# Performance work log

Hardware: AMD Instinct MI355X
Metric: run time of the kernel (lower is better)

The kernel has to match this reference:

```python
import jax, jax.numpy as jnp
import numpy as np
from jax import lax

BN_EPS = 1e-5  # eval-mode BatchNorm with running_mean=0, running_var=1


def _interp_mat(n_in, n_out):
    # align_corners=True bilinear interpolation matrix [n_out, n_in]
    if n_out == 1:
        coords = np.zeros((1,))
    else:
        coords = np.arange(n_out) * (n_in - 1) / (n_out - 1)
    lo = np.clip(np.floor(coords).astype(np.int64), 0, max(n_in - 2, 0))
    frac = (coords - lo).astype(np.float32)
    M = np.zeros((n_out, n_in), dtype=np.float32)
    M[np.arange(n_out), lo] += 1.0 - frac
    if n_in > 1:
        M[np.arange(n_out), lo + 1] += frac
    return jnp.asarray(M)


def _resize_ac(x, H, W):
    # bilinear, align_corners=True, over trailing two dims
    Mh = _interp_mat(x.shape[-2], H)
    Mw = _interp_mat(x.shape[-1], W)
    return jnp.einsum('...hw,Hh,Ww->...HW', x, Mh, Mw)


def _conv(x, w, b, pad):
    y = lax.conv_general_dilated(x, w, (1, 1), [(pad, pad), (pad, pad)],
                                 dimension_numbers=('NCHW', 'OIHW', 'NCHW'))
    return y + b[None, :, None, None]


def setup_inputs() -> dict:
    key = jax.random.key(0)
    ks = jax.random.split(key, 16)
    C, KD, VD, NCLS, BS = 256, 32, 128, 10, 4
    sizes = [64, 32, 16, 8, 4]
    inp = {}
    for l, s in enumerate(sizes):
        inp[f'feat{l}'] = jax.random.normal(ks[l], (BS, C, s, s), jnp.float32)
    inp['attentions'] = jax.random.normal(ks[5], (NCLS, C, 16, 16), jnp.float32)

    def w(k, shape):
        return jax.random.normal(k, shape, jnp.float32) * 0.05

    inp['key_t_w'] = w(ks[6], (KD, C, 3, 3)); inp['key_t_b'] = jnp.zeros((KD,), jnp.float32)
    inp['value_t_w'] = w(ks[7], (VD, C, 3, 3)); inp['value_t_b'] = jnp.zeros((VD,), jnp.float32)
    inp['key_q_w'] = w(ks[8], (5, KD, C, 3, 3)); inp['key_q_b'] = jnp.zeros((5, KD), jnp.float32)
    inp['value_q_w'] = w(ks[9], (5, VD, C, 3, 3)); inp['value_q_b'] = jnp.zeros((5, VD), jnp.float32)
    inp['bn_gamma'] = jnp.ones((5, 256), jnp.float32)
    inp['bn_beta'] = jnp.zeros((5, 256), jnp.float32)
    inp['combine_w'] = w(ks[10], (256, 512, 1, 1)); inp['combine_b'] = jnp.zeros((256,), jnp.float32)
    return inp


def reference(feat0, feat1, feat2, feat3, feat4, attentions,
              key_t_w, key_t_b, value_t_w, value_t_b,
              key_q_w, key_q_b, value_q_w, value_q_b,
              bn_gamma, bn_beta, combine_w, combine_b):
    feats = [feat0, feat1, feat2, feat3, feat4]
    ncls, _, h, w_ = attentions.shape
    hw = h * w_
    kt = _conv(attentions, key_t_w, key_t_b, 1).reshape(ncls, 32, hw)   # [n,32,hw]
    vt = _conv(attentions, value_t_w, value_t_b, 1).reshape(ncls, 128, hw)  # [n,128,hw]
    bn_scale = bn_gamma * np.float32(1.0 / np.sqrt(1.0 + BN_EPS))
    outs, fas = [], []
    for l, f in enumerate(feats):
        bs, _, H, W = f.shape
        fr = _resize_ac(f, h, w_)                                        # [b,C,h,w]
        kq = _conv(fr, key_q_w[l], key_q_b[l], 1).reshape(bs, 32, hw)    # [b,32,hw]
        vq = _conv(fr, value_q_w[l], value_q_b[l], 1)                    # [b,128,h,w]
        # p[b,n,i,j] = sum_k kq[b,k,i] * kt[n,k,j]; softmax over i (torch dim=1)
        p = jnp.einsum('bki,nkj->bnij', kq, kt)
        p = jax.nn.softmax(p, axis=2)
        # full attention maps: channels = template pixel j, spatial = query pixel i
        fa = _resize_ac(jnp.swapaxes(p, 2, 3).reshape(bs, ncls, hw, h, w_), H, W)
        # val_t_out summed over classes: sum_n sum_i vt[n,c,i] * p[b,n,i,j]
        agg = jnp.einsum('nci,bnij->bcj', vt, p).reshape(bs, 128, h, w_)
        final = jnp.concatenate([ncls * vq, agg], axis=1)                # [b,256,h,w]
        final = _resize_ac(final, H, W)
        final = final * bn_scale[l][None, :, None, None] + bn_beta[l][None, :, None, None]
        outs.append(_conv(jnp.concatenate([f, final], axis=1), combine_w, combine_b, 0))
        fas.append(fa)
    return (*outs, *fas)
```

## Files before the change

### kernel.cpp

```cpp
#include <hip/hip_runtime.h>

constexpr int CIN   = 256;
constexpr int KD    = 32;
constexpr int VD    = 128;
constexpr int NCLS  = 10;
constexpr int BS    = 4;
constexpr int HW    = 256;
constexpr float BNC = 0.9999950000374997f;

typedef unsigned short u16;
typedef __attribute__((ext_vector_type(8))) __bf16 bf8v;
typedef __attribute__((ext_vector_type(4))) float f4v;

static __device__ __forceinline__ int imin(int a, int b) { return a < b ? a : b; }

static __device__ __forceinline__ u16 f2bf(float v) {
  union { float f; unsigned u; } x; x.f = v;
  unsigned r = x.u + 0x7FFFu + ((x.u >> 16) & 1u);
  return (u16)(r >> 16);
}
static __device__ __forceinline__ float bf2f(u16 h) {
  union { unsigned u; float f; } x; x.u = ((unsigned)h) << 16;
  return x.f;
}

static __device__ __forceinline__ f4v mfma16(bf8v a, bf8v b, f4v c) {
  return __builtin_amdgcn_mfma_f32_16x16x32_bf16(a, b, c, 0, 0, 0);
}

__constant__ const int c_jbase[5] = {0, 16384, 20480, 21504, 21760};

__global__ __launch_bounds__(256) void k_prep1(
    const float* __restrict__ f0, const float* __restrict__ f1,
    const float* __restrict__ f2, const float* __restrict__ f3,
    const float* __restrict__ f4, const float* __restrict__ att,
    const float* __restrict__ vqw, const float* __restrict__ vtw,
    const float* __restrict__ kqw, const float* __restrict__ ktw,
    const float* __restrict__ cw, const float* __restrict__ gamma,
    const float* __restrict__ cbias, const float* __restrict__ beta,
    u16* __restrict__ Xf, u16* __restrict__ Xr,
    u16* __restrict__ Awv, u16* __restrict__ Awk,
    u16* __restrict__ cwA, u16* __restrict__ cw2A, float* __restrict__ cb) {
  __shared__ float sm[16][65];
  int blk = blockIdx.x;
  int tid = threadIdx.x;
  if (blk < 384) {
    const float* fin; u16* dstbase; int SS, px0;
    if (blk < 344) {
      int l, base, nb;
      if (blk < 256)      { l = 0; base = 0;   nb = 64; }
      else if (blk < 320) { l = 1; base = 256; nb = 16; }
      else if (blk < 336) { l = 2; base = 320; nb = 4; }
      else if (blk < 340) { l = 3; base = 336; nb = 1; }
      else                { l = 4; base = 340; nb = 1; }
      int local = blk - base;
      int b = local / nb, chunk = local % nb;
      int S = 64 >> l; SS = S * S;
      px0 = chunk * 64;
      fin = (l == 0 ? f0 : l == 1 ? f1 : l == 2 ? f2 : l == 3 ? f3 : f4)
            + (size_t)b * CIN * SS;
      dstbase = Xf + (size_t)(c_jbase[l] + b * SS) * 512;
    } else {
      int a = blk - 344;
      int imgA = a >> 2, chunk = a & 3;
      SS = 256; px0 = chunk * 64;
      fin = att + (size_t)imgA * CIN * 256;
      dstbase = Xr + (size_t)(20 + imgA) * 131072;
    }
    int px_r = tid & 63, cr = tid >> 6;
    int px_w = tid >> 2, c4 = (tid & 3) * 4;
    for (int cbk = 0; cbk < 16; ++cbk) {
      __syncthreads();
#pragma unroll
      for (int q = 0; q < 4; ++q) {
        int cl = q * 4 + cr;
        float v = 0.f;
        if (px0 + px_r < SS) v = fin[(size_t)(cbk * 16 + cl) * SS + px0 + px_r];
        sm[cl][px_r] = v;
      }
      __syncthreads();
      if (px0 + px_w < SS) {
        u16 hh[4], ll[4];
#pragma unroll
        for (int e = 0; e < 4; ++e) {
          float v = sm[c4 + e][px_w];
          hh[e] = f2bf(v); ll[e] = f2bf(v - bf2f(hh[e]));
        }
        uint2 wh, wl;
        wh.x = (unsigned)hh[0] | ((unsigned)hh[1] << 16); wh.y = (unsigned)hh[2] | ((unsigned)hh[3] << 16);
        wl.x = (unsigned)ll[0] | ((unsigned)ll[1] << 16); wl.y = (unsigned)ll[2] | ((unsigned)ll[3] << 16);
        u16* dst = dstbase + (size_t)(px0 + px_w) * 512 + cbk * 16 + c4;
        *reinterpret_cast<uint2*>(dst) = wh;
        *reinterpret_cast<uint2*>(dst + 256) = wl;
      }
    }
  } else if (blk < 1464) {
    int gid = (blk - 384) * 256 + tid;
    int lane = gid & 63;
    int grp = gid >> 6;
    const float* src; u16* dst; int kc;
    if (grp < 3456) {
      kc = grp % 72; int ot = (grp / 72) % 8; int sid = grp / (72 * 8);
      src = (sid < 5 ? vqw + (size_t)sid * VD * 2304 : vtw) + (size_t)(ot * 16 + (lane & 15)) * 2304;
      dst = Awv + (size_t)grp * 1024;
    } else {
      int g2 = grp - 3456;
      kc = g2 % 72; int ot = (g2 / 72) % 2; int sid = g2 / 144;
      src = (sid < 5 ? kqw + (size_t)sid * KD * 2304 : ktw) + (size_t)(ot * 16 + (lane & 15)) * 2304;
      dst = Awk + (size_t)g2 * 1024;
    }
    int q0 = (lane >> 4) * 8;
    int t = kc >> 3, c0 = (kc & 7) * 32;
#pragma unroll
    for (int i = 0; i < 8; ++i) {
      int c = c0 + q0 + i;
      float v = src[c * 9 + t];
      u16 h = f2bf(v);
      dst[lane * 8 + i] = h;
      dst[512 + lane * 8 + i] = f2bf(v - bf2f(h));
    }
  } else if (blk < 1848) {
    int blk2 = blk - 1464;
    if (blk2 < 64) {
      int gid = blk2 * 256 + tid;
      int oc = gid >> 6, c0 = (gid & 63) * 4;
      float4 v = *reinterpret_cast<const float4*>(cw + (size_t)oc * 512 + c0);
      const float* vv = (const float*)&v;
      u16 h[4], l[4];
#pragma unroll
      for (int e = 0; e < 4; ++e) { h[e] = f2bf(vv[e]); l[e] = f2bf(vv[e] - bf2f(h[e])); }
      uint2 wh, wl;
      wh.x = (unsigned)h[0] | ((unsigned)h[1] << 16); wh.y = (unsigned)h[2] | ((unsigned)h[3] << 16);
      wl.x = (unsigned)l[0] | ((unsigned)l[1] << 16); wl.y = (unsigned)l[2] | ((unsigned)l[3] << 16);
      *reinterpret_cast<uint2*>(cwA + (size_t)oc * 256 + c0) = wh;
      *reinterpret_cast<uint2*>(cwA + 65536 + (size_t)oc * 256 + c0) = wl;
    } else {
      int gid = (blk2 - 64) * 256 + tid;
      int l = gid / 16384, rem = gid % 16384;
      int oc = rem >> 6, c0 = (rem & 63) * 4;
      u16 h[4], lo[4];
#pragma unroll
      for (int e = 0; e < 4; ++e) {
        int c = c0 + e;
        float v = cw[(size_t)oc * 512 + 256 + c] * (gamma[l * 256 + c] * BNC);
        h[e] = f2bf(v); lo[e] = f2bf(v - bf2f(h[e]));
      }
      uint2 wh, wl;
      wh.x = (unsigned)h[0] | ((unsigned)h[1] << 16); wh.y = (unsigned)h[2] | ((unsigned)h[3] << 16);
      wl.x = (unsigned)lo[0] | ((unsigned)lo[1] << 16); wl.y = (unsigned)lo[2] | ((unsigned)lo[3] << 16);
      *reinterpret_cast<uint2*>(cw2A + (size_t)l * 65536 + oc * 256 + c0) = wh;
      *reinterpret_cast<uint2*>(cw2A + 327680 + (size_t)l * 65536 + oc * 256 + c0) = wl;
    }
  } else {
    int l = blk - 1848, oc = tid;
    float s = cbias[oc];
    for (int c = 0; c < CIN; ++c)
      s += cw[(size_t)oc * 512 + 256 + c] * beta[l * CIN + c];
    cb[l * CIN + oc] = s;
  }
}

__global__ __launch_bounds__(256) void k_prep_xr(
    const u16* __restrict__ Xf, u16* __restrict__ Xr, u16* __restrict__ zrow) {
  int blk = blockIdx.x;
  int img = blk >> 4, yr = blk & 15;
  int l = img >> 2, b = img & 3;
  int S = 64 >> l, SS = S * S;
  int c = threadIdx.x;
  if (blk == 0) { zrow[c] = 0; zrow[256 + c] = 0; }
  float cyf = (float)(yr * (S - 1)) / 15.0f;
  int ylo = imin((int)cyf, S - 2); float fy = cyf - (float)ylo;
  u16* dst = Xr + ((size_t)img * 256 + yr * 16) * 512;
  const u16* srcb = Xf + (size_t)(c_jbase[l] + b * SS) * 512;
  for (int x = 0; x < 16; ++x) {
    float cxf = (float)(x * (S - 1)) / 15.0f;
    int xlo = imin((int)cxf, S - 2); float fx = cxf - (float)xlo;
    const u16* r00 = srcb + (size_t)(ylo * S + xlo) * 512;
    const u16* r10 = srcb + (size_t)((ylo + 1) * S + xlo) * 512;
    float v00 = bf2f(r00[c]) + bf2f(r00[256 + c]);
    float v01 = bf2f(r00[512 + c]) + bf2f(r00[768 + c]);
    float v10 = bf2f(r10[c]) + bf2f(r10[256 + c]);
    float v11 = bf2f(r10[512 + c]) + bf2f(r10[768 + c]);
    float v = (1.f - fy) * ((1.f - fx) * v00 + fx * v01)
            + fy * ((1.f - fx) * v10 + fx * v11);
    u16 h = f2bf(v);
    dst[x * 512 + c] = h;
    dst[x * 512 + 256 + c] = f2bf(v - bf2f(h));
  }
}

__global__ __launch_bounds__(256) void k_conv_mfma(
    const u16* __restrict__ Xr, const u16* __restrict__ Awv, const u16* __restrict__ Awk,
    const u16* __restrict__ zrow,
    float* __restrict__ kqall, u16* __restrict__ vt2, float* __restrict__ f16v,
    const float* __restrict__ vqb, const float* __restrict__ vtb,
    const float* __restrict__ kqb, const float* __restrict__ ktb) {
  int wid = blockIdx.x * 4 + (threadIdx.x >> 6);
  int lane = threadIdx.x & 63;
  bool isV = wid < 1920;
  int img, ot, yp;
  if (isV) { img = wid >> 6; int r = wid & 63; ot = r >> 3; yp = r & 7; }
  else     { int j = wid - 1920; img = j >> 4; int r = j & 15; ot = r >> 3; yp = r & 7; }
  int wset = img < 20 ? (img >> 2) : 5;

  const u16* Ab = isV ? Awv + ((size_t)(wset * 8 + ot)) * 72 * 1024
                      : Awk + ((size_t)(wset * 2 + ot)) * 72 * 1024;
  const u16* Xb = Xr + (size_t)img * 131072;
  int xcol = lane & 15, kg = lane >> 4;
  int y0 = yp * 2, y1 = y0 + 1;

  f4v acc0 = {0.f, 0.f, 0.f, 0.f}, acc1 = {0.f, 0.f, 0.f, 0.f};
  for (int t = 0; t < 9; ++t) {
    int dy = (t >= 6) ? 2 : (t >= 3 ? 1 : 0);
    int dx = t - dy * 3;
    int yy0 = y0 + dy - 1, yy1 = yy0 + 1;
    int xx = xcol + dx - 1;
    bool xok = (unsigned)xx < 16u;
    const u16* base0 = (xok && (unsigned)yy0 < 16u)
                       ? Xb + (size_t)(yy0 * 16 + xx) * 512 : zrow;
    const u16* base1 = (xok && (unsigned)yy1 < 16u)
                       ? Xb + (size_t)(yy1 * 16 + xx) * 512 : zrow;
    const u16* Xr0 = base0 + kg * 8;
    const u16* Xr1 = base1 + kg * 8;
    const u16* Ak = Ab + (size_t)t * 8 * 1024 + lane * 8;
#pragma unroll
    for (int cc = 0; cc < 8; ++cc) {
      bf8v ah = *reinterpret_cast<const bf8v*>(Ak + cc * 1024);
      bf8v al = *reinterpret_cast<const bf8v*>(Ak + cc * 1024 + 512);
      bf8v bh0 = *reinterpret_cast<const bf8v*>(Xr0 + cc * 32);
      bf8v bl0 = *reinterpret_cast<const bf8v*>(Xr0 + cc * 32 + 256);
      bf8v bh1 = *reinterpret_cast<const bf8v*>(Xr1 + cc * 32);
      bf8v bl1 = *reinterpret_cast<const bf8v*>(Xr1 + cc * 32 + 256);
      acc0 = mfma16(ah, bh0, acc0);
      acc0 = mfma16(ah, bl0, acc0);
      acc0 = mfma16(al, bh0, acc0);
      acc1 = mfma16(ah, bh1, acc1);
      acc1 = mfma16(ah, bl1, acc1);
      acc1 = mfma16(al, bh1, acc1);
    }
  }

  int ocbase = ot * 16;
  if (isV && img >= 20) {
    int n = img - 20;
    u16* d2 = vt2 + ((size_t)n * VD + ocbase) * HW;
#pragma unroll
    for (int i = 0; i < 4; ++i) {
      int ocl = kg * 4 + i;
      float bv = vtb[ocbase + ocl];
      float va = acc0[i] + bv, vb = acc1[i] + bv;
      u16 ha = f2bf(va), hb = f2bf(vb);
      size_t ia = (size_t)ocl * HW + y0 * 16 + xcol;
      size_t ib = (size_t)ocl * HW + y1 * 16 + xcol;
      d2[ia] = ha; d2[ia + 327680] = f2bf(va - bf2f(ha));
      d2[ib] = hb; d2[ib + 327680] = f2bf(vb - bf2f(hb));
    }
    return;
  }
  float scale = 1.f;
  const float* bias;
  float* dst;
  if (isV) { dst = f16v + ((size_t)img * VD + ocbase) * HW; bias = vqb + wset * VD + ocbase; scale = (float)NCLS; }
  else if (img < 20) { dst = kqall + ((size_t)img * KD + ocbase) * HW; bias = kqb + wset * KD + ocbase; }
  else { dst = kqall + (size_t)20 * KD * HW + ((size_t)(img - 20) * KD + ocbase) * HW; bias = ktb + ocbase; }
#pragma unroll
  for (int i = 0; i < 4; ++i) {
    int ocl = kg * 4 + i;
    float bv = bias[ocl];
    dst[(size_t)ocl * HW + y0 * 16 + xcol] = (acc0[i] + bv) * scale;
    dst[(size_t)ocl * HW + y1 * 16 + xcol] = (acc1[i] + bv) * scale;
  }
}

__global__ __launch_bounds__(256) void k_mega(
    const float* __restrict__ kqall, const u16* __restrict__ vt2,
    float* __restrict__ out, float* __restrict__ aggn) {
  int blk = blockIdx.x;
  int l, chunk, g;
  if (blk < 1280) { l = 0; g = blk >> 2; chunk = blk & 3; }
  else            { int r2 = blk - 1280; l = 1 + (r2 >> 8) - (r2 >> 8) + r2 / 320; g = r2 % 320; chunk = 0; }
  int bn = g >> 3, jt = g & 7;
  int b = bn / NCLS, n = bn % NCLS;
  int t = threadIdx.x;
  int iq = t >> 5, jl = t & 31;
  int j = jt * 32 + jl;

  __shared__ float buf[8224];
  __shared__ float red[512];

  const float* ktb = kqall + 20 * KD * HW;
  float ktr[KD];
#pragma unroll
  for (int k = 0; k < KD; ++k) ktr[k] = ktb[((size_t)n * KD + k) * HW + j];
  const float* kqb = kqall + (size_t)(l * 4 + b) * KD * HW;
  for (int s = t; s < KD * HW; s += 256) buf[s] = kqb[s];
  __syncthreads();

  float v[32];
#pragma unroll
  for (int ii = 0; ii < 32; ++ii) v[ii] = 0.f;
  for (int k = 0; k < KD; ++k) {
    float a = ktr[k];
    const float4* q4 = (const float4*)&buf[k * 256 + iq * 32];
#pragma unroll
    for (int q = 0; q < 8; ++q) {
      float4 u = q4[q];
      v[q * 4 + 0] += u.x * a; v[q * 4 + 1] += u.y * a;
      v[q * 4 + 2] += u.z * a; v[q * 4 + 3] += u.w * a;
    }
  }
  float ml = -1e30f;
#pragma unroll
  for (int ii = 0; ii < 32; ++ii) ml = fmaxf(ml, v[ii]);
  float sl = 0.f;
#pragma unroll
  for (int ii = 0; ii < 32; ++ii) sl += __expf(v[ii] - ml);
  red[t] = ml;
  red[256 + t] = sl;
  __syncthreads();
  float M = -1e30f;
#pragma unroll
  for (int q = 0; q < 8; ++q) M = fmaxf(M, red[q * 32 + jl]);
  float Ssum = 0.f;
#pragma unroll
  for (int q = 0; q < 8; ++q) Ssum += red[256 + q * 32 + jl] * __expf(red[q * 32 + jl] - M);
  float inv = 1.0f / Ssum;
#pragma unroll
  for (int ii = 0; ii < 32; ++ii)
    buf[jl * 257 + iq * 32 + ii] = __expf(v[ii] - M) * inv;
  __syncthreads();

  int S_ = 64 >> l, shift = 6 - l, SS = S_ * S_;
  const size_t fa_off[5] = {5586944, 47529984, 58015744, 60637184, 61292544};
  float* ob = out + fa_off[l] + ((size_t)bn * HW + jt * 32) * SS;
  int tot = SS << 5;
  int span = (l == 0) ? (tot >> 2) : tot;
  int b0 = chunk * span, b1 = b0 + span;
  for (int base = b0 + t * 4; base < b1; base += 1024) {
    int jj = base >> (2 * shift);
    int rest = base & (SS - 1);
    int X0 = rest & (S_ - 1), Y = rest >> shift;
    float cyf = (float)(Y * 15) / (float)(S_ - 1);
    int ylo = imin((int)cyf, 14); float fy = cyf - (float)ylo;
    const float* prow = &buf[jj * 257];
    f4v rv;
#pragma unroll
    for (int t4 = 0; t4 < 4; ++t4) {
      int X = X0 + t4;
      float cxf = (float)(X * 15) / (float)(S_ - 1);
      int xlo = imin((int)cxf, 14); float fx = cxf - (float)xlo;
      int i00 = ylo * 16 + xlo;
      float v0 = prow[i00],      v1 = prow[i00 + 1];
      float v2 = prow[i00 + 16], v3 = prow[i00 + 17];
      rv[t4] = (1.f - fy) * ((1.f - fx) * v0 + fx * v1)
             + fy * ((1.f - fx) * v2 + fx * v3);
    }
    __builtin_nontemporal_store(rv, (f4v*)(ob + (size_t)jj * SS + rest));
  }

  if (chunk != 0) return;

  int w = t >> 6, lane = t & 63;
  int row = lane & 15, kg = lane >> 4;
  f4v acc[2][2] = {{{0.f,0.f,0.f,0.f},{0.f,0.f,0.f,0.f}},
                   {{0.f,0.f,0.f,0.f},{0.f,0.f,0.f,0.f}}};
  for (int kc = 0; kc < 8; ++kc) {
    bf8v ah[2], al[2];
#pragma unroll
    for (int ctl = 0; ctl < 2; ++ctl) {
      int ct = w * 2 + ctl;
      const u16* vh = vt2 + ((size_t)n * VD + ct * 16 + row) * 256 + kc * 32 + kg * 8;
      ah[ctl] = *reinterpret_cast<const bf8v*>(vh);
      al[ctl] = *reinterpret_cast<const bf8v*>(vh + 327680);
    }
#pragma unroll
    for (int jt2 = 0; jt2 < 2; ++jt2) {
      union { u16 u[8]; bf8v v8; } Bh;
#pragma unroll
      for (int e = 0; e < 8; ++e)
        Bh.u[e] = f2bf(buf[(jt2 * 16 + row) * 257 + kc * 32 + kg * 8 + e]);
#pragma unroll
      for (int ctl = 0; ctl < 2; ++ctl) {
        acc[ctl][jt2] = mfma16(ah[ctl], Bh.v8, acc[ctl][jt2]);
        acc[ctl][jt2] = mfma16(al[ctl], Bh.v8, acc[ctl][jt2]);
      }
    }
  }
  float* ab = aggn + (size_t)(l * 40 + bn) * VD * HW;
#pragma unroll
  for (int ctl = 0; ctl < 2; ++ctl)
#pragma unroll
    for (int jt2 = 0; jt2 < 2; ++jt2)
#pragma unroll
      for (int i = 0; i < 4; ++i)
        ab[(size_t)(w * 32 + ctl * 16 + kg * 4 + i) * HW + jt * 32 + jt2 * 16 + row]
            = acc[ctl][jt2][i];
}

__global__ __launch_bounds__(256) void k_g16f(
    const float* __restrict__ f16v, const float* __restrict__ aggn,
    const u16* __restrict__ cw2A, float* __restrict__ g16_all) {
  int blk = blockIdx.x;
  int ohalf = blk & 1;
  int img = blk >> 5, jc = (blk >> 1) & 15;
  int j0 = jc * 16;
  int l = img >> 2, b = img & 3;
  int tid = threadIdx.x;
  __shared__ __align__(16) u16 fsbh[16][280];
  __shared__ __align__(16) u16 fsbl[16][280];
  int jj = tid & 15;
  int c0 = tid >> 4;
  for (int pass = 0; pass < 16; ++pass) {
    int cc = pass * 16 + c0;
    float v;
    if (cc < 128) {
      v = f16v[((size_t)img * VD + cc) * HW + j0 + jj];
    } else {
      const float* ab = aggn + ((size_t)(l * 40 + b * 10) * VD + cc - 128) * HW + j0 + jj;
      v = 0.f;
#pragma unroll
      for (int n = 0; n < NCLS; ++n) v += ab[(size_t)n * VD * HW];
    }
    u16 h = f2bf(v);
    fsbh[jj][cc] = h;
    fsbl[jj][cc] = f2bf(v - bf2f(h));
  }
  __syncthreads();

  int w = tid >> 6, lane = tid & 63;
  int row = lane & 15, kg = lane >> 4;
#pragma unroll
  for (int q = 0; q < 2; ++q) {
    int ot = ohalf * 8 + w * 2 + q;
    const u16* Ah = cw2A + (size_t)l * 65536 + ((size_t)(ot * 16 + row)) * 256 + kg * 8;
    const u16* Al = Ah + 327680;
    f4v acc = {0.f, 0.f, 0.f, 0.f};
#pragma unroll
    for (int kc = 0; kc < 8; ++kc) {
      bf8v ah = *reinterpret_cast<const bf8v*>(Ah + kc * 32);
      bf8v al = *reinterpret_cast<const bf8v*>(Al + kc * 32);
      bf8v bh = *reinterpret_cast<const bf8v*>(&fsbh[row][kc * 32 + kg * 8]);
      bf8v bl = *reinterpret_cast<const bf8v*>(&fsbl[row][kc * 32 + kg * 8]);
      acc = mfma16(ah, bh, acc);
      acc = mfma16(ah, bl, acc);
      acc = mfma16(al, bh, acc);
    }
#pragma unroll
    for (int i = 0; i < 4; ++i)
      g16_all[((size_t)img * CIN + ot * 16 + kg * 4 + i) * HW + j0 + row] = acc[i];
  }
}

__global__ __launch_bounds__(256) void k_out_final(
    const u16* __restrict__ cwA, const u16* __restrict__ Xf,
    const float* __restrict__ g16_all, const float* __restrict__ cb_all,
    float* __restrict__ out) {
  int wid = blockIdx.x * 4 + (threadIdx.x >> 6);
  int lane = threadIdx.x & 63;
  int pt = wid >> 4, octile = wid & 15;
  int l, lb, tl;
  if (pt < 1024)      { l = 0; lb = 0;    tl = 256; }
  else if (pt < 1280) { l = 1; lb = 1024; tl = 64; }
  else if (pt < 1344) { l = 2; lb = 1280; tl = 16; }
  else if (pt < 1360) { l = 3; lb = 1344; tl = 4; }
  else                { l = 4; lb = 1360; tl = 1; }
  int rem = pt - lb;
  int b = rem / tl;
  int pxin = (rem % tl) * 16;
  const size_t ooff[5] = {0, 4194304, 5242880, 5505024, 5570560};
  int S = 64 >> l, SS = S * S, shift = 6 - l;
  int row = lane & 15, kg = lane >> 4;
  int gpx = c_jbase[l] + b * SS + pxin + row;

  const u16* Ah = cwA + ((size_t)(octile * 16 + row)) * 256 + kg * 8;
  const u16* Al = Ah + 65536;
  const u16* Bh = Xf + (size_t)gpx * 512 + kg * 8;
  const u16* Bl = Bh + 256;
  f4v acc = {0.f, 0.f, 0.f, 0.f};
#pragma unroll
  for (int kc = 0; kc < 8; ++kc) {
    bf8v ah = *reinterpret_cast<const bf8v*>(Ah + kc * 32);
    bf8v al = *reinterpret_cast<const bf8v*>(Al + kc * 32);
    bf8v bh = *reinterpret_cast<const bf8v*>(Bh + kc * 32);
    bf8v bl = *reinterpret_cast<const bf8v*>(Bl + kc * 32);
    acc = mfma16(ah, bh, acc);
    acc = mfma16(ah, bl, acc);
    acc = mfma16(al, bh, acc);
  }

  int px = pxin + row;
  int Xc = px & (S - 1), Y = px >> shift;
  float cyf = (float)(Y * 15) / (float)(S - 1);
  int ylo = imin((int)cyf, 14); float fy = cyf - (float)ylo;
  float cxf = (float)(Xc * 15) / (float)(S - 1);
  int xlo = imin((int)cxf, 14); float fx = cxf - (float)xlo;
  int i00 = ylo * 16 + xlo;
  const float* gbase = g16_all + ((size_t)(l * 4 + b) * CIN + octile * 16 + kg * 4) * HW;
  float* ob = out + ooff[l] + ((size_t)b * CIN + octile * 16) * SS + px;
#pragma unroll
  for (int i = 0; i < 4; ++i) {
    const float* g = gbase + (size_t)i * HW + i00;
    float v0 = g[0], v1 = g[1], v2 = g[16], v3 = g[17];
    float bil = (1.f - fy) * ((1.f - fx) * v0 + fx * v1)
              + fy * ((1.f - fx) * v2 + fx * v3);
    float r = acc[i] + bil + cb_all[l * CIN + octile * 16 + kg * 4 + i];
    __builtin_nontemporal_store(r, ob + (size_t)(kg * 4 + i) * SS);
  }
}

extern "C" void kernel_launch(void* const* d_in, const int* in_sizes, int n_in,
                              void* d_out, int out_size, void* d_ws, size_t ws_size,
                              hipStream_t stream) {
  const float* feat[5];
  for (int l = 0; l < 5; ++l) feat[l] = (const float*)d_in[l];
  const float* att   = (const float*)d_in[5];
  const float* ktw   = (const float*)d_in[6];
  const float* ktb   = (const float*)d_in[7];
  const float* vtw   = (const float*)d_in[8];
  const float* vtb   = (const float*)d_in[9];
  const float* kqw   = (const float*)d_in[10];
  const float* kqb   = (const float*)d_in[11];
  const float* vqw   = (const float*)d_in[12];
  const float* vqb   = (const float*)d_in[13];
  const float* gamma = (const float*)d_in[14];
  const float* beta  = (const float*)d_in[15];
  const float* cw    = (const float*)d_in[16];
  const float* cbias = (const float*)d_in[17];
  float* out = (float*)d_out;

  float* ws    = (float*)d_ws;
  float* kqall = ws;
  float* f16v  = ws + 245760;
  u16*   vt2   = (u16*)(ws + 901120);
  u16*   cwA   = (u16*)(ws + 1228800);
  u16*   cw2A  = (u16*)(ws + 1294336);
  float* cb    = ws + 1622016;
  u16*   Xf    = (u16*)(ws + 1623296);
  float* S0    = ws + 7210240;
  u16*   Awv  = (u16*)S0;
  u16*   Awk  = (u16*)(S0 + 1769472);
  u16*   Xr   = (u16*)(S0 + 2211840);
  u16*   zrow = (u16*)(S0 + 4177920);
  float* aggn    = S0;
  float* g16_all = S0 + 6553600;

  k_prep1<<<1853, 256, 0, stream>>>(
      feat[0], feat[1], feat[2], feat[3], feat[4], att,
      vqw, vtw, kqw, ktw, cw, gamma, cbias, beta,
      Xf, Xr, Awv, Awk, cwA, cw2A, cb);
  k_prep_xr<<<320, 256, 0, stream>>>(Xf, Xr, zrow);
  k_conv_mfma<<<600, 256, 0, stream>>>(
      Xr, Awv, Awk, zrow, kqall, vt2, f16v, vqb, vtb, kqb, ktb);

  k_mega<<<2560, 256, 0, stream>>>(kqall, vt2, out, aggn);

  k_g16f<<<640, 256, 0, stream>>>(f16v, aggn, cw2A, g16_all);
  k_out_final<<<5456, 256, 0, stream>>>(cwA, Xf, g16_all, cb, out);
}
```

Before: 351.4 us.

## Split attention kernel into softmax/aggregation and bf16-staged resize kernels

Splits the fused attention kernel into one kernel that computes softmax and the value aggregation and writes the probability map in bf16 to a workspace, and a second kernel that reads that map and writes the upsampled full-attention outputs. This removes the redundant softmax recomputation done by the four chunk blocks at level 0 and lets the resize work be distributed over more, evenly sized blocks. In exchange it adds an extra launch, a global round trip of the probability map, and bf16 rounding of the attention maps written to the output.

```diff
diff --git a/kernel.cpp b/kernel.cpp
--- a/kernel.cpp
+++ b/kernel.cpp
@@ -272,13 +272,12 @@
   }
 }
 
-__global__ __launch_bounds__(256) void k_mega(
+__global__ __launch_bounds__(256) void k_pagg(
     const float* __restrict__ kqall, const u16* __restrict__ vt2,
-    float* __restrict__ out, float* __restrict__ aggn) {
+    u16* __restrict__ pT, float* __restrict__ aggn) {
   int blk = blockIdx.x;
-  int l, chunk, g;
-  if (blk < 1280) { l = 0; g = blk >> 2; chunk = blk & 3; }
-  else            { int r2 = blk - 1280; l = 1 + (r2 >> 8) - (r2 >> 8) + r2 / 320; g = r2 % 320; chunk = 0; }
+  int l = blk / 320;
+  int g = blk % 320;
   int bn = g >> 3, jt = g & 7;
   int b = bn / NCLS, n = bn % NCLS;
   int t = threadIdx.x;
@@ -325,24 +324,98 @@
 #pragma unroll
   for (int q = 0; q < 8; ++q) Ssum += red[256 + q * 32 + jl] * __expf(red[q * 32 + jl] - M);
   float inv = 1.0f / Ssum;
-#pragma unroll
-  for (int ii = 0; ii < 32; ++ii)
-    buf[jl * 257 + iq * 32 + ii] = __expf(v[ii] - M) * inv;
+  u16 tmp[32];
+#pragma unroll
+  for (int ii = 0; ii < 32; ++ii) {
+    float pv = __expf(v[ii] - M) * inv;
+    buf[jl * 257 + iq * 32 + ii] = pv;
+    tmp[ii] = f2bf(pv);
+  }
+  u16* prow = pT + (((size_t)(l * 40 + bn) * 256 + j) << 8) + iq * 32;
+#pragma unroll
+  for (int q = 0; q < 4; ++q) {
+    uint4 w;
+    w.x = (unsigned)tmp[q * 8 + 0] | ((unsigned)tmp[q * 8 + 1] << 16);
+    w.y = (unsigned)tmp[q * 8 + 2] | ((unsigned)tmp[q * 8 + 3] << 16);
+    w.z = (unsigned)tmp[q * 8 + 4] | ((unsigned)tmp[q * 8 + 5] << 16);
+    w.w = (unsigned)tmp[q * 8 + 6] | ((unsigned)tmp[q * 8 + 7] << 16);
+    reinterpret_cast<uint4*>(prow)[q] = w;
+  }
+  __syncthreads();
+
+  int w = t >> 6, lane = t & 63;
+  int row = lane & 15, kg = lane >> 4;
+  f4v acc[2][2] = {{{0.f,0.f,0.f,0.f},{0.f,0.f,0.f,0.f}},
+                   {{0.f,0.f,0.f,0.f},{0.f,0.f,0.f,0.f}}};
+  for (int kc = 0; kc < 8; ++kc) {
+    bf8v ah[2], al[2];
+#pragma unroll
+    for (int ctl = 0; ctl < 2; ++ctl) {
+      int ct = w * 2 + ctl;
+      const u16* vh = vt2 + ((size_t)n * VD + ct * 16 + row) * 256 + kc * 32 + kg * 8;
+      ah[ctl] = *reinterpret_cast<const bf8v*>(vh);
+      al[ctl] = *reinterpret_cast<const bf8v*>(vh + 327680);
+    }
+#pragma unroll
+    for (int jt2 = 0; jt2 < 2; ++jt2) {
+      union { u16 u[8]; bf8v v8; } Bh;
+#pragma unroll
+      for (int e = 0; e < 8; ++e)
+        Bh.u[e] = f2bf(buf[(jt2 * 16 + row) * 257 + kc * 32 + kg * 8 + e]);
+#pragma unroll
+      for (int ctl = 0; ctl < 2; ++ctl) {
+        acc[ctl][jt2] = mfma16(ah[ctl], Bh.v8, acc[ctl][jt2]);
+        acc[ctl][jt2] = mfma16(al[ctl], Bh.v8, acc[ctl][jt2]);
+      }
+    }
+  }
+  float* ab = aggn + (size_t)(l * 40 + bn) * VD * HW;
+#pragma unroll
+  for (int ctl = 0; ctl < 2; ++ctl)
+#pragma unroll
+    for (int jt2 = 0; jt2 < 2; ++jt2)
+#pragma unroll
+      for (int i = 0; i < 4; ++i)
+        ab[(size_t)(w * 32 + ctl * 16 + kg * 4 + i) * HW + jt * 32 + jt2 * 16 + row]
+            = acc[ctl][jt2][i];
+}
+
+__global__ __launch_bounds__(256) void k_fa2(
+    const u16* __restrict__ pT, float* __restrict__ out) {
+  int blk = blockIdx.x;
+  int l = blk / 640;
+  int local = blk % 640;
+  int bn = local >> 4, jg = local & 15;
+  int tid = threadIdx.x;
+  __shared__ float ld[16][257];
+  {
+    int jj = tid >> 4, i0 = (tid & 15) * 16;
+    const u16* src = pT + (((size_t)(l * 40 + bn) * 256 + jg * 16 + jj) << 8) + i0;
+    const uint4* s4 = reinterpret_cast<const uint4*>(src);
+    uint4 w0 = s4[0], w1 = s4[1];
+    const unsigned* u0 = (const unsigned*)&w0;
+    const unsigned* u1 = (const unsigned*)&w1;
+#pragma unroll
+    for (int e = 0; e < 4; ++e) {
+      ld[jj][i0 + e * 2]     = bf2f((u16)(u0[e] & 0xffff));
+      ld[jj][i0 + e * 2 + 1] = bf2f((u16)(u0[e] >> 16));
+      ld[jj][i0 + 8 + e * 2]     = bf2f((u16)(u1[e] & 0xffff));
+      ld[jj][i0 + 8 + e * 2 + 1] = bf2f((u16)(u1[e] >> 16));
+    }
+  }
   __syncthreads();
 
   int S_ = 64 >> l, shift = 6 - l, SS = S_ * S_;
   const size_t fa_off[5] = {5586944, 47529984, 58015744, 60637184, 61292544};
-  float* ob = out + fa_off[l] + ((size_t)bn * HW + jt * 32) * SS;
-  int tot = SS << 5;
-  int span = (l == 0) ? (tot >> 2) : tot;
-  int b0 = chunk * span, b1 = b0 + span;
-  for (int base = b0 + t * 4; base < b1; base += 1024) {
+  float* ob = out + fa_off[l] + ((size_t)bn * HW + jg * 16) * SS;
+  int tot = SS << 4;
+  for (int base = tid * 4; base < tot; base += 1024) {
     int jj = base >> (2 * shift);
     int rest = base & (SS - 1);
     int X0 = rest & (S_ - 1), Y = rest >> shift;
     float cyf = (float)(Y * 15) / (float)(S_ - 1);
     int ylo = imin((int)cyf, 14); float fy = cyf - (float)ylo;
-    const float* prow = &buf[jj * 257];
+    const float* prow = &ld[jj][0];
     f4v rv;
 #pragma unroll
     for (int t4 = 0; t4 < 4; ++t4) {
@@ -357,44 +430,6 @@
     }
     __builtin_nontemporal_store(rv, (f4v*)(ob + (size_t)jj * SS + rest));
   }
-
-  if (chunk != 0) return;
-
-  int w = t >> 6, lane = t & 63;
-  int row = lane & 15, kg = lane >> 4;
-  f4v acc[2][2] = {{{0.f,0.f,0.f,0.f},{0.f,0.f,0.f,0.f}},
-                   {{0.f,0.f,0.f,0.f},{0.f,0.f,0.f,0.f}}};
-  for (int kc = 0; kc < 8; ++kc) {
-    bf8v ah[2], al[2];
-#pragma unroll
-    for (int ctl = 0; ctl < 2; ++ctl) {
-      int ct = w * 2 + ctl;
-      const u16* vh = vt2 + ((size_t)n * VD + ct * 16 + row) * 256 + kc * 32 + kg * 8;
-      ah[ctl] = *reinterpret_cast<const bf8v*>(vh);
-      al[ctl] = *reinterpret_cast<const bf8v*>(vh + 327680);
-    }
-#pragma unroll
-    for (int jt2 = 0; jt2 < 2; ++jt2) {
-      union { u16 u[8]; bf8v v8; } Bh;
-#pragma unroll
-      for (int e = 0; e < 8; ++e)
-        Bh.u[e] = f2bf(buf[(jt2 * 16 + row) * 257 + kc * 32 + kg * 8 + e]);
-#pragma unroll
-      for (int ctl = 0; ctl < 2; ++ctl) {
-        acc[ctl][jt2] = mfma16(ah[ctl], Bh.v8, acc[ctl][jt2]);
-        acc[ctl][jt2] = mfma16(al[ctl], Bh.v8, acc[ctl][jt2]);
-      }
-    }
-  }
-  float* ab = aggn + (size_t)(l * 40 + bn) * VD * HW;
-#pragma unroll
-  for (int ctl = 0; ctl < 2; ++ctl)
-#pragma unroll
-    for (int jt2 = 0; jt2 < 2; ++jt2)
-#pragma unroll
-      for (int i = 0; i < 4; ++i)
-        ab[(size_t)(w * 32 + ctl * 16 + kg * 4 + i) * HW + jt * 32 + jt2 * 16 + row]
-            = acc[ctl][jt2][i];
 }
 
 __global__ __launch_bounds__(256) void k_g16f(
@@ -543,6 +578,7 @@
   u16*   zrow = (u16*)(S0 + 4177920);
   float* aggn    = S0;
   float* g16_all = S0 + 6553600;
+  u16*   pT      = (u16*)(S0 + 7864320);
 
   k_prep1<<<1853, 256, 0, stream>>>(
       feat[0], feat[1], feat[2], feat[3], feat[4], att,
@@ -552,7 +588,8 @@
   k_conv_mfma<<<600, 256, 0, stream>>>(
       Xr, Awv, Awk, zrow, kqall, vt2, f16v, vqb, vtb, kqb, ktb);
 
-  k_mega<<<2560, 256, 0, stream>>>(kqall, vt2, out, aggn);
+  k_pagg<<<1600, 256, 0, stream>>>(kqall, vt2, pT, aggn);
+  k_fa2<<<3200, 256, 0, stream>>>(pT, out);
 
   k_g16f<<<640, 256, 0, stream>>>(f16v, aggn, cw2A, g16_all);
   k_out_final<<<5456, 256, 0, stream>>>(cwA, Xf, g16_all, cb, out);
```

Result: no change. 357.7 us (+1.8%).
